# Optimization experiments

Hardware: AMD Instinct MI355X
Metric: run time of the kernel (lower is better)

The kernel has to match this reference:

```python
import jax, jax.numpy as jnp
import numpy as np

TOKENS = 8192
IN_F = 4096
OUT_F = 11008


def setup_inputs() -> dict:
    key = jax.random.key(0)
    k1, k2, k3, k4, k5 = jax.random.split(key, 5)
    x = jax.random.normal(k1, (TOKENS, IN_F), dtype=jnp.float32)
    # packed int4 weights: one int32 byte-value in [0,256) per pair of int4s
    weight_packed = jax.random.randint(k2, (IN_F, OUT_F // 2), 0, 256, dtype=jnp.int32)
    weight_scale = jax.random.uniform(k3, (OUT_F,), dtype=jnp.float32) * 0.02 + 1e-3
    weight_offset = jax.random.normal(k4, (OUT_F,), dtype=jnp.float32)  # stored as -offset, as in module
    bias = jax.random.normal(k5, (OUT_F,), dtype=jnp.float32)
    return {"x": x, "weight_packed": weight_packed, "weight_scale": weight_scale,
            "weight_offset": weight_offset, "bias": bias}


def _unpack_int4(weight_packed):
    # inverse of int42int8: low nibble = even column, high nibble = odd column,
    # both signed int4 in [-8, 7]. Sign-extend via (v ^ 8) - 8.
    low = ((weight_packed & 15) ^ 8) - 8
    high = (((weight_packed >> 4) & 15) ^ 8) - 8
    k = weight_packed.shape[0]
    q = jnp.stack([low, high], axis=-1).reshape(k, -1)  # [in, out]
    return q


def reference(x, weight_packed, weight_scale, weight_offset, bias):
    q = _unpack_int4(weight_packed).astype(jnp.float32)          # [in, out]
    w = (q + weight_offset[None, :]) * weight_scale[None, :]      # dequant: stored offset is -zero_point
    return x @ w + bias[None, :]                                  # [tokens, out]
```

## Files before the change

kernel.cpp:

```cpp
#include <hip/hip_runtime.h>
#include <stdint.h>

#define TOKENS 8192
#define IN_F   4096
#define OUT_F  11008
#define PACKED (OUT_F / 2)
#define NKT    (IN_F / 64)

typedef __bf16   bf16x8 __attribute__((ext_vector_type(8)));
typedef float    f32x4  __attribute__((ext_vector_type(4)));
typedef uint16_t u16x8  __attribute__((ext_vector_type(8)));

__device__ __forceinline__ uint16_t f32_to_bf16(float f) {
    union { float f; uint32_t u; } c; c.f = f;
    uint32_t r = c.u + 0x7FFFu + ((c.u >> 16) & 1u);
    return (uint16_t)(r >> 16);
}

__global__ __launch_bounds__(256) void xcvt_kernel(const float* __restrict__ x,
                                                   uint16_t* __restrict__ xb) {
    size_t base = ((size_t)blockIdx.x * 256 + threadIdx.x) * 8;
    float4 v0 = *(const float4*)(x + base);
    float4 v1 = *(const float4*)(x + base + 4);
    u16x8 o;
    o[0] = f32_to_bf16(v0.x); o[1] = f32_to_bf16(v0.y);
    o[2] = f32_to_bf16(v0.z); o[3] = f32_to_bf16(v0.w);
    o[4] = f32_to_bf16(v1.x); o[5] = f32_to_bf16(v1.y);
    o[6] = f32_to_bf16(v1.z); o[7] = f32_to_bf16(v1.w);
    *(u16x8*)(xb + base) = o;
}

#define WDQ_STRIDE 72
__global__ __launch_bounds__(256) void wdeq_kernel(const int* __restrict__ wp,
                                                   const float* __restrict__ woff,
                                                   uint16_t* __restrict__ wt) {
    __shared__ uint16_t tile[64 * WDQ_STRIDE];
    const int t  = threadIdx.x;
    const int p0 = blockIdx.y * 32;
    const int k0 = blockIdx.x * 64;
    const int pl = t & 31;
    const int kb = t >> 5;
    const int p  = p0 + pl;
    const float off_e = woff[2 * p];
    const float off_o = woff[2 * p + 1];
    #pragma unroll
    for (int j = 0; j < 8; ++j) {
        int kl = j * 8 + kb;
        int v  = wp[(size_t)(k0 + kl) * PACKED + p];
        int lo = ((v & 15) ^ 8) - 8;
        int hi = (((v >> 4) & 15) ^ 8) - 8;
        tile[(2 * pl)     * WDQ_STRIDE + kl] = f32_to_bf16((float)lo + off_e);
        tile[(2 * pl + 1) * WDQ_STRIDE + kl] = f32_to_bf16((float)hi + off_o);
    }
    __syncthreads();
    const int nl = t >> 2;
    const int kc = (t & 3) * 16;
    u16x8 w0 = *(const u16x8*)&tile[nl * WDQ_STRIDE + kc];
    u16x8 w1 = *(const u16x8*)&tile[nl * WDQ_STRIDE + kc + 8];
    uint16_t* dst = wt + (size_t)(2 * p0 + nl) * IN_F + k0 + kc;
    *(u16x8*)dst       = w0;
    *(u16x8*)(dst + 8) = w1;
}


#define CP16(ldsp, gp)                                                                        \
    __builtin_amdgcn_global_load_lds((const __attribute__((address_space(1))) void*)(gp),     \
                                     (__attribute__((address_space(3))) void*)(ldsp), 16, 0, 0)

#define STAGE2(ldsoff, gptr) {                                      \
    CP16((char*)smem + (ldsoff),        (gptr));                    \
    CP16((char*)smem + (ldsoff) + 8192, (gptr) + 262144); }

#define FENCE() asm volatile("" ::: "memory")
#define BAR()  { FENCE(); __builtin_amdgcn_s_barrier(); FENCE(); }

#define LDA(MH) {                                                       \
    _Pragma("unroll") for (int im = 0; im < 4; ++im) {                  \
      a[im][0] = *(const bf16x8*)(Ard + ((MH)*4+im)*2048 + swz0);       \
      a[im][1] = *(const bf16x8*)(Ard + ((MH)*4+im)*2048 + swz1); } }

#define LDB(dst, NH) {                                                  \
    _Pragma("unroll") for (int i2 = 0; i2 < 2; ++i2) {                  \
      dst[i2][0] = *(const bf16x8*)(Brd + ((NH)*2+i2)*2048 + swz0);     \
      dst[i2][1] = *(const bf16x8*)(Brd + ((NH)*2+i2)*2048 + swz1); } }

#define MMA(MH, NH, B) {                                                \
    __builtin_amdgcn_s_setprio(1);                                      \
    _Pragma("unroll") for (int ik = 0; ik < 2; ++ik)                    \
      _Pragma("unroll") for (int im = 0; im < 4; ++im)                  \
        _Pragma("unroll") for (int i2 = 0; i2 < 2; ++i2)                \
          acc[(MH)*4+im][(NH)*2+i2] = __builtin_amdgcn_mfma_f32_16x16x32_bf16( \
              a[im][ik], B[i2][ik], acc[(MH)*4+im][(NH)*2+i2], 0, 0, 0); \
    __builtin_amdgcn_s_setprio(0); }

__global__ __launch_bounds__(512, 2) void gemm_kernel(const uint16_t* __restrict__ xb,
                                                      const uint16_t* __restrict__ wt,
                                                      const float* __restrict__ scale,
                                                      const float* __restrict__ bias,
                                                      float* __restrict__ out) {
    __shared__ char smem[131072];

    const int tid  = threadIdx.x;
    const int w    = tid >> 6;
    const int lane = tid & 63;
    const int quad = lane >> 4;
    const int l15  = lane & 15;
    const int wm   = w >> 2;
    const int wn   = w & 3;

    const int bm = blockIdx.x & 31;
    const int bn = blockIdx.x >> 5;
    const int m0 = bm << 8;
    const int n0 = bn << 8;

    const int srow = tid >> 3;
    const int schk = (tid & 7) ^ (srow & 7);
    const uint16_t* gA = xb + (size_t)(m0 + srow) * IN_F + schk * 8;
    const uint16_t* gB = wt + (size_t)(n0 + srow) * IN_F + schk * 8;
    const int wb = w * 1024;

    const int swz0 = (( quad     ) ^ (l15 & 7)) * 16 + l15 * 128;
    const int swz1 = ((quad + 4) ^ (l15 & 7)) * 16 + l15 * 128;

    const char* lds = (const char*)smem;

    STAGE2(65536 +                 wb, gB);
    STAGE2(65536 + 16384 +         wb, gB + 524288);
    STAGE2(                        wb, gA);
    STAGE2(16384 +                 wb, gA + 524288);
    STAGE2(65536 + 32768 +         wb, gB + 64);
    STAGE2(65536 + 32768 + 16384 + wb, gB + 64 + 524288);
    asm volatile("s_waitcnt vmcnt(4)" ::: "memory");
    BAR();

    f32x4  acc[8][4] = {};
    bf16x8 a[4][2], b0[2][2], b1[2][2];

    #pragma unroll 2
    for (int kt = 0; kt < NKT; ++kt) {
        const int p = kt & 1;
        const char* Ard = lds + p * 32768 + wm * 16384;
        const char* Brd = lds + 65536 + p * 32768 + (wn >> 1) * 16384 + (wn & 1) * 8192;
        const int AstB = (p ^ 1) * 32768 + wb;
        const int BstB = 65536 + p * 32768 + wb;
        const bool stA = kt < NKT - 1;
        const bool stB = kt < NKT - 2;

        LDA(0); LDB(b0, 0);
        if (stA) STAGE2(AstB, gA + 64);
        BAR();
        MMA(0, 0, b0);
        BAR();
        LDB(b1, 1);
        if (stA) STAGE2(AstB + 16384, gA + 64 + 524288);
        BAR();
        MMA(0, 1, b1);
        BAR();
        LDA(1);
        if (stB) STAGE2(BstB, gB + 128);
        BAR();
        MMA(1, 1, b1);
        BAR();
        if (stB) STAGE2(BstB + 16384, gB + 128 + 524288);
        if (kt < NKT - 2)       { asm volatile("s_waitcnt vmcnt(4)" ::: "memory"); }
        else if (kt == NKT - 2) { asm volatile("s_waitcnt vmcnt(0)" ::: "memory"); }
        BAR();
        MMA(1, 0, b0);
        BAR();

        gA += 64; gB += 64;
    }

    #pragma unroll
    for (int nf = 0; nf < 4; ++nf) {
        const int n    = n0 + wn * 64 + nf * 16 + l15;
        const float s  = scale[n];
        const float bb = bias[n];
        #pragma unroll
        for (int mf = 0; mf < 8; ++mf) {
            const int m = m0 + wm * 128 + mf * 16 + quad * 4;
            float* o = out + (size_t)m * OUT_F + n;
            #pragma unroll
            for (int r = 0; r < 4; ++r)
                o[(size_t)r * OUT_F] = acc[mf][nf][r] * s + bb;
        }
    }
}

extern "C" void kernel_launch(void* const* d_in, const int* in_sizes, int n_in,
                              void* d_out, int out_size, void* d_ws, size_t ws_size,
                              hipStream_t stream) {
    const float* x     = (const float*)d_in[0];
    const int*   wp    = (const int*)d_in[1];
    const float* scale = (const float*)d_in[2];
    const float* woff  = (const float*)d_in[3];
    const float* bias  = (const float*)d_in[4];
    float* out = (float*)d_out;

    uint16_t* xb = (uint16_t*)d_ws;
    uint16_t* wt = xb + (size_t)TOKENS * IN_F;

    xcvt_kernel<<<(TOKENS * (size_t)IN_F) / (256 * 8), 256, 0, stream>>>(x, xb);
    wdeq_kernel<<<dim3(IN_F / 64, PACKED / 32), 256, 0, stream>>>(wp, woff, wt);
    gemm_kernel<<<(TOKENS / 256) * (OUT_F / 256), 512, 0, stream>>>(xb, wt, scale, bias, out);
}
```

Baseline: 1.137 ms.

## Switch GEMM inner loop to 32x32x16 bf16 MFMA with restructured LDS reads

Replaces the 16x16x32 bf16 MFMA tiles with 32x32x16 MFMA instructions. This changes the per-wave fragment layout, the swizzled LDS read offsets, the accumulator shape and the epilogue index mapping. The k-loop is also manually unrolled by two tiles with explicit tail handling, and both B fragments are loaded up front. Larger MFMA tiles mean fewer LDS fragment reads and instructions per FLOP, at the cost of more registers and a changed schedule.

```diff
diff --git a/kernel.cpp b/kernel.cpp
--- a/kernel.cpp
+++ b/kernel.cpp
@@ -8,7 +8,7 @@
 #define NKT    (IN_F / 64)
 
 typedef __bf16   bf16x8 __attribute__((ext_vector_type(8)));
-typedef float    f32x4  __attribute__((ext_vector_type(4)));
+typedef float    f32x16 __attribute__((ext_vector_type(16)));
 typedef uint16_t u16x8  __attribute__((ext_vector_type(8)));
 
 __device__ __forceinline__ uint16_t f32_to_bf16(float f) {
@@ -74,24 +74,62 @@
 #define FENCE() asm volatile("" ::: "memory")
 #define BAR()  { FENCE(); __builtin_amdgcn_s_barrier(); FENCE(); }
 
-#define LDA(MH) {                                                       \
-    _Pragma("unroll") for (int im = 0; im < 4; ++im) {                  \
-      a[im][0] = *(const bf16x8*)(Ard + ((MH)*4+im)*2048 + swz0);       \
-      a[im][1] = *(const bf16x8*)(Ard + ((MH)*4+im)*2048 + swz1); } }
-
-#define LDB(dst, NH) {                                                  \
-    _Pragma("unroll") for (int i2 = 0; i2 < 2; ++i2) {                  \
-      dst[i2][0] = *(const bf16x8*)(Brd + ((NH)*2+i2)*2048 + swz0);     \
-      dst[i2][1] = *(const bf16x8*)(Brd + ((NH)*2+i2)*2048 + swz1); } }
-
-#define MMA(MH, NH, B) {                                                \
-    __builtin_amdgcn_s_setprio(1);                                      \
-    _Pragma("unroll") for (int ik = 0; ik < 2; ++ik)                    \
-      _Pragma("unroll") for (int im = 0; im < 4; ++im)                  \
-        _Pragma("unroll") for (int i2 = 0; i2 < 2; ++i2)                \
-          acc[(MH)*4+im][(NH)*2+i2] = __builtin_amdgcn_mfma_f32_16x16x32_bf16( \
-              a[im][ik], B[i2][ik], acc[(MH)*4+im][(NH)*2+i2], 0, 0, 0); \
+#define VM4 asm volatile("s_waitcnt vmcnt(4)" ::: "memory");
+#define VM0 asm volatile("s_waitcnt vmcnt(0)" ::: "memory");
+#define VMX
+
+#define LDA(MH) {                                                        \
+    _Pragma("unroll") for (int im = 0; im < 2; ++im) {                   \
+      const char* ap = Ard + ((MH)*2+im)*4096 + rowb;                    \
+      a[im][0] = *(const bf16x8*)(ap + sz0);                             \
+      a[im][1] = *(const bf16x8*)(ap + sz1);                             \
+      a[im][2] = *(const bf16x8*)(ap + sz2);                             \
+      a[im][3] = *(const bf16x8*)(ap + sz3); } }
+
+#define LDB(dst, NH) {                                                   \
+    { const char* bp = Brd + (NH)*4096 + rowb;                           \
+      dst[0] = *(const bf16x8*)(bp + sz0);                               \
+      dst[1] = *(const bf16x8*)(bp + sz1);                               \
+      dst[2] = *(const bf16x8*)(bp + sz2);                               \
+      dst[3] = *(const bf16x8*)(bp + sz3); } }
+
+#define MMA(MH, NH, B) {                                                 \
+    __builtin_amdgcn_s_setprio(1);                                       \
+    _Pragma("unroll") for (int ks = 0; ks < 4; ++ks)                     \
+      _Pragma("unroll") for (int im = 0; im < 2; ++im)                   \
+        acc[(MH)*2+im][NH] = __builtin_amdgcn_mfma_f32_32x32x16_bf16(    \
+            a[im][ks], B[ks], acc[(MH)*2+im][NH], 0, 0, 0);              \
     __builtin_amdgcn_s_setprio(0); }
+
+#define KTILE(P, STA, STB, VMN) {                                        \
+    const char* Ard = lds + (P)*32768 + wm*16384;                        \
+    const char* Brd = lds + 65536 + (P)*32768 + bsel;                    \
+                                                                 \
+    LDA(0);                                                              \
+    LDB(b0, 0);                                                          \
+    LDB(b1, 1);                            \
+    if (STA) STAGE2(((P)^1)*32768 + wb, gA + 64);                        \
+    BAR();                                                               \
+    MMA(0, 0, b0);                                                       \
+    BAR();                                                               \
+                                                                 \
+    if (STA) STAGE2(((P)^1)*32768 + 16384 + wb, gA + 64 + 262144*2);     \
+    BAR();                                                               \
+    MMA(0, 1, b1);                                                       \
+    LDA(1);                          \
+    BAR();                                                               \
+                                                                 \
+    if (STB) STAGE2(65536 + (P)*32768 + wb, gB + 128);                   \
+    BAR();                                                               \
+    MMA(1, 1, b1);                                                       \
+    BAR();                                                               \
+                                                                 \
+    if (STB) STAGE2(65536 + (P)*32768 + 16384 + wb, gB + 128 + 262144*2);\
+    VMN                                                                  \
+    BAR();                                                               \
+    MMA(1, 0, b0);                                                       \
+    BAR();                                                               \
+    gA += 64; gB += 64; }
 
 __global__ __launch_bounds__(512, 2) void gemm_kernel(const uint16_t* __restrict__ xb,
                                                       const uint16_t* __restrict__ wt,
@@ -103,8 +141,8 @@
     const int tid  = threadIdx.x;
     const int w    = tid >> 6;
     const int lane = tid & 63;
-    const int quad = lane >> 4;
-    const int l15  = lane & 15;
+    const int l31  = lane & 31;
+    const int hi   = lane >> 5;
     const int wm   = w >> 2;
     const int wn   = w & 3;
 
@@ -119,70 +157,48 @@
     const uint16_t* gB = wt + (size_t)(n0 + srow) * IN_F + schk * 8;
     const int wb = w * 1024;
 
-    const int swz0 = (( quad     ) ^ (l15 & 7)) * 16 + l15 * 128;
-    const int swz1 = ((quad + 4) ^ (l15 & 7)) * 16 + l15 * 128;
+    const int rowb = l31 * 128;
+    const int x7   = l31 & 7;
+    const int sz0 = ((0 + hi) ^ x7) * 16;
+    const int sz1 = ((2 + hi) ^ x7) * 16;
+    const int sz2 = ((4 + hi) ^ x7) * 16;
+    const int sz3 = ((6 + hi) ^ x7) * 16;
+    const int bsel = (wn >> 1) * 16384 + (wn & 1) * 8192;
 
     const char* lds = (const char*)smem;
 
     STAGE2(65536 +                 wb, gB);
-    STAGE2(65536 + 16384 +         wb, gB + 524288);
+    STAGE2(65536 + 16384 +         wb, gB + 262144*2);
     STAGE2(                        wb, gA);
-    STAGE2(16384 +                 wb, gA + 524288);
+    STAGE2(16384 +                 wb, gA + 262144*2);
     STAGE2(65536 + 32768 +         wb, gB + 64);
-    STAGE2(65536 + 32768 + 16384 + wb, gB + 64 + 524288);
-    asm volatile("s_waitcnt vmcnt(4)" ::: "memory");
+    STAGE2(65536 + 32768 + 16384 + wb, gB + 64 + 262144*2);
+    VM4
     BAR();
 
-    f32x4  acc[8][4] = {};
-    bf16x8 a[4][2], b0[2][2], b1[2][2];
-
-    #pragma unroll 2
-    for (int kt = 0; kt < NKT; ++kt) {
-        const int p = kt & 1;
-        const char* Ard = lds + p * 32768 + wm * 16384;
-        const char* Brd = lds + 65536 + p * 32768 + (wn >> 1) * 16384 + (wn & 1) * 8192;
-        const int AstB = (p ^ 1) * 32768 + wb;
-        const int BstB = 65536 + p * 32768 + wb;
-        const bool stA = kt < NKT - 1;
-        const bool stB = kt < NKT - 2;
-
-        LDA(0); LDB(b0, 0);
-        if (stA) STAGE2(AstB, gA + 64);
-        BAR();
-        MMA(0, 0, b0);
-        BAR();
-        LDB(b1, 1);
-        if (stA) STAGE2(AstB + 16384, gA + 64 + 524288);
-        BAR();
-        MMA(0, 1, b1);
-        BAR();
-        LDA(1);
-        if (stB) STAGE2(BstB, gB + 128);
-        BAR();
-        MMA(1, 1, b1);
-        BAR();
-        if (stB) STAGE2(BstB + 16384, gB + 128 + 524288);
-        if (kt < NKT - 2)       { asm volatile("s_waitcnt vmcnt(4)" ::: "memory"); }
-        else if (kt == NKT - 2) { asm volatile("s_waitcnt vmcnt(0)" ::: "memory"); }
-        BAR();
-        MMA(1, 0, b0);
-        BAR();
-
-        gA += 64; gB += 64;
+    f32x16 acc[4][2] = {};
+    bf16x8 a[2][4], b0[4], b1[4];
+
+    for (int kt2 = 0; kt2 < 31; ++kt2) {
+        KTILE(0, 1, 1, VM4)
+        KTILE(1, 1, 1, VM4)
     }
+    KTILE(0, 1, 0, VM0)
+    KTILE(1, 0, 0, VMX)
 
     #pragma unroll
-    for (int nf = 0; nf < 4; ++nf) {
-        const int n    = n0 + wn * 64 + nf * 16 + l15;
+    for (int nt = 0; nt < 2; ++nt) {
+        const int n    = n0 + wn * 64 + nt * 32 + l31;
         const float s  = scale[n];
         const float bb = bias[n];
         #pragma unroll
-        for (int mf = 0; mf < 8; ++mf) {
-            const int m = m0 + wm * 128 + mf * 16 + quad * 4;
-            float* o = out + (size_t)m * OUT_F + n;
+        for (int mt = 0; mt < 4; ++mt) {
+            const int mbase = m0 + wm * 128 + mt * 32 + 4 * hi;
             #pragma unroll
-            for (int r = 0; r < 4; ++r)
-                o[(size_t)r * OUT_F] = acc[mf][nf][r] * s + bb;
+            for (int r = 0; r < 16; ++r) {
+                const int m = mbase + (r & 3) + 8 * (r >> 2);
+                out[(size_t)m * OUT_F + n] = acc[mt][nt][r] * s + bb;
+            }
         }
     }
 }
```

New measurement: 1.192 ms. 4.9% more time.

## Vectorize int4 dequant with float-bit tricks and remap GEMM blocks per XCD

Applied to the files above, without the earlier changes.

The weight dequant kernel now has each thread load 8 consecutive K rows and build floats through an exponent-bias bit trick instead of integer sign extension. It packs pairs into bf16 with v_cvt_pk_bf16_f32 and writes 16-byte vector stores to LDS in place of scalar 2-byte stores. The GEMM grid index is remapped so that consecutive blocks on each of the 8 XCDs cover contiguous tiles, which should improve L2 reuse of A and B. The bit trick depends on exact float arithmetic for small integers, and the remap assumes 1376 blocks divide evenly across 8 XCDs.

```diff
diff --git a/kernel.cpp b/kernel.cpp
--- a/kernel.cpp
+++ b/kernel.cpp
@@ -10,11 +10,15 @@
 typedef __bf16   bf16x8 __attribute__((ext_vector_type(8)));
 typedef float    f32x4  __attribute__((ext_vector_type(4)));
 typedef uint16_t u16x8  __attribute__((ext_vector_type(8)));
+typedef uint32_t u32x4  __attribute__((ext_vector_type(4)));
 
 __device__ __forceinline__ uint16_t f32_to_bf16(float f) {
     union { float f; uint32_t u; } c; c.f = f;
     uint32_t r = c.u + 0x7FFFu + ((c.u >> 16) & 1u);
     return (uint16_t)(r >> 16);
+}
+__device__ __forceinline__ float u2f(uint32_t u) {
+    union { uint32_t u; float f; } c; c.u = u; return c.f;
 }
 
 __global__ __launch_bounds__(256) void xcvt_kernel(const float* __restrict__ x,
@@ -41,17 +45,28 @@
     const int pl = t & 31;
     const int kb = t >> 5;
     const int p  = p0 + pl;
-    const float off_e = woff[2 * p];
-    const float off_o = woff[2 * p + 1];
+    const int kl0 = kb * 8;
+    float2 of = *(const float2*)(woff + 2 * p);
+    const float cE = of.x - 136.0f;
+    const float cO = of.y - 136.0f;
+    int v[8];
     #pragma unroll
-    for (int j = 0; j < 8; ++j) {
-        int kl = j * 8 + kb;
-        int v  = wp[(size_t)(k0 + kl) * PACKED + p];
-        int lo = ((v & 15) ^ 8) - 8;
-        int hi = (((v >> 4) & 15) ^ 8) - 8;
-        tile[(2 * pl)     * WDQ_STRIDE + kl] = f32_to_bf16((float)lo + off_e);
-        tile[(2 * pl + 1) * WDQ_STRIDE + kl] = f32_to_bf16((float)hi + off_o);
+    for (int j = 0; j < 8; ++j) v[j] = wp[(size_t)(k0 + kl0 + j) * PACKED + p];
+    uint32_t dl[4], dh[4];
+    #pragma unroll
+    for (int j = 0; j < 4; ++j) {
+        int a = v[2 * j], b = v[2 * j + 1];
+        float fl0 = u2f(0x43080000u ^ ((uint32_t)(a & 15) << 16)) + cE;
+        float fl1 = u2f(0x43080000u ^ ((uint32_t)(b & 15) << 16)) + cE;
+        float fh0 = u2f(0x43080000u ^ ((uint32_t)(a & 0xF0) << 12)) + cO;
+        float fh1 = u2f(0x43080000u ^ ((uint32_t)(b & 0xF0) << 12)) + cO;
+        asm("v_cvt_pk_bf16_f32 %0, %1, %2" : "=v"(dl[j]) : "v"(fl0), "v"(fl1));
+        asm("v_cvt_pk_bf16_f32 %0, %1, %2" : "=v"(dh[j]) : "v"(fh0), "v"(fh1));
     }
+    u32x4 wl = { dl[0], dl[1], dl[2], dl[3] };
+    u32x4 wh = { dh[0], dh[1], dh[2], dh[3] };
+    *(u32x4*)&tile[(2 * pl)     * WDQ_STRIDE + kl0] = wl;
+    *(u32x4*)&tile[(2 * pl + 1) * WDQ_STRIDE + kl0] = wh;
     __syncthreads();
     const int nl = t >> 2;
     const int kc = (t & 3) * 16;
@@ -108,8 +123,10 @@
     const int wm   = w >> 2;
     const int wn   = w & 3;
 
-    const int bm = blockIdx.x & 31;
-    const int bn = blockIdx.x >> 5;
+    const int orig = blockIdx.x;
+    const int wg   = (orig & 7) * 172 + (orig >> 3);
+    const int bm = wg & 31;
+    const int bn = wg >> 5;
     const int m0 = bm << 8;
     const int n0 = bn << 8;
 
@@ -119,7 +136,7 @@
     const uint16_t* gB = wt + (size_t)(n0 + srow) * IN_F + schk * 8;
     const int wb = w * 1024;
 
-    const int swz0 = (( quad     ) ^ (l15 & 7)) * 16 + l15 * 128;
+    const int swz0 = ((quad    ) ^ (l15 & 7)) * 16 + l15 * 128;
     const int swz1 = ((quad + 4) ^ (l15 & 7)) * 16 + l15 * 128;
 
     const char* lds = (const char*)smem;
```

New measurement: 1.174 ms. 3.3% more time.
